# Performance work log

Measured on AMD Instinct MI355X. Metric: run time of the kernel, lower is better.

## Reference

```python
import jax, jax.numpy as jnp
import numpy as np

N, E, D, H, G, C = 100000, 1200000, 64, 64, 128, 10


def setup_inputs() -> dict:
    key = jax.random.key(0)
    ks = jax.random.split(key, 20)
    def lin(k, fin, fout):
        kw, kb = jax.random.split(k)
        s = 1.0 / np.sqrt(fin)
        return (jax.random.uniform(kw, (fin, fout), jnp.float32, -s, s),
                jax.random.uniform(kb, (fout,), jnp.float32, -s, s))
    w1a, b1a = lin(ks[0], D, H)
    w1b, b1b = lin(ks[1], H, H)
    w2a, b2a = lin(ks[2], H, H)
    w2b, b2b = lin(ks[3], H, H)
    w3a, b3a = lin(ks[4], H, H)
    w3b, b3b = lin(ks[5], H, H)
    wc, bc = lin(ks[6], H, C)
    x = jax.random.normal(ks[7], (N, D), jnp.float32)
    edge_index = jax.random.randint(ks[8], (2, E), 0, N, dtype=jnp.int32)
    batch = jnp.sort(jax.random.randint(ks[9], (N,), 0, G, dtype=jnp.int32))
    return {"x": x, "w1a": w1a, "b1a": b1a, "w1b": w1b, "b1b": b1b,
            "w2a": w2a, "b2a": b2a, "w2b": w2b, "b2b": b2b,
            "w3a": w3a, "b3a": b3a, "w3b": w3b, "b3b": b3b,
            "wc": wc, "bc": bc, "edge_index": edge_index, "batch": batch}


def _gin_layer(x, src, dst, wa, ba, wb, bb):
    # GINConv (eps=0): mlp(x + sum_{j in N(i)} x_j), then outer ReLU from GIN.forward
    agg = jax.ops.segment_sum(x[src], dst, num_segments=N)  # [N, d]
    h = x + agg
    h = jax.nn.relu(h @ wa + ba) @ wb + bb
    return jax.nn.relu(h)


def reference(x, w1a, b1a, w1b, b1b, w2a, b2a, w2b, b2b,
              w3a, b3a, w3b, b3b, wc, bc, edge_index, batch):
    src, dst = edge_index[0], edge_index[1]
    x = _gin_layer(x, src, dst, w1a, b1a, w1b, b1b)
    x = _gin_layer(x, src, dst, w2a, b2a, w2b, b2b)
    x = _gin_layer(x, src, dst, w3a, b3a, w3b, b3b)
    # global mean pool over graphs
    sums = jax.ops.segment_sum(x, batch, num_segments=G)              # [G, H]
    cnts = jax.ops.segment_sum(jnp.ones((N,), x.dtype), batch, num_segments=G)
    pooled = sums / jnp.maximum(cnts, 1.0)[:, None]
    return pooled @ wc + bc  # [G, C]
```

## Files before the change

### kernel.cpp

```cpp
#include <hip/hip_runtime.h>
#include <hip/hip_bf16.h>


#define N_NODES 100000
#define N_EDGES 1200000
#define N_GRAPH 128
#define N_CLS   10
#define NBUCK   391
#define BCAP    4096
#define BSH     12

typedef __bf16 bf16_t;
typedef __bf16 bf16x8 __attribute__((ext_vector_type(8)));
typedef float  f32x4  __attribute__((ext_vector_type(4)));

__global__ void tobf_kernel(const float* __restrict__ x, bf16_t* __restrict__ xb,
                            int* __restrict__ bcnt, float* __restrict__ gsum,
                            const float* __restrict__ w1a, const float* __restrict__ w1b,
                            const float* __restrict__ w2a, const float* __restrict__ w2b,
                            const float* __restrict__ w3a, const float* __restrict__ w3b,
                            bf16_t* __restrict__ wfragG,
                            bf16_t* __restrict__ hPad, bf16_t* __restrict__ xAPad) {
    const int tid = threadIdx.x;
    if (blockIdx.x == 0) {
        for (int i = tid; i < NBUCK; i += 256) bcnt[i] = 0;
    } else if (blockIdx.x == 1) {
        f32x4* g4 = (f32x4*)gsum;
        for (int i = tid; i < N_GRAPH * 16; i += 256)
            g4[i] = (f32x4){0.f, 0.f, 0.f, 0.f};
        if (tid < 64) {
            xb[N_NODES * 64 + tid]    = (bf16_t)0.f;
            hPad[N_NODES * 64 + tid]  = (bf16_t)0.f;
            xAPad[N_NODES * 64 + tid] = (bf16_t)0.f;
        }
    } else if (blockIdx.x <= 4) {
        const int L = blockIdx.x - 2;
        const float* wA = L == 0 ? w1a : (L == 1 ? w2a : w3a);
        const float* wB = L == 0 ? w1b : (L == 1 ? w2b : w3b);
        const int k  = tid >> 2;
        const int n0 = (tid & 3) << 4;
        const int ks = k >> 5, qd = (k >> 3) & 3, jj = k & 7;
        const int fi = ((n0 >> 4) << 1) + ks;
#pragma unroll
        for (int m = 0; m < 2; ++m) {
            const float* w = m ? wB : wA;
            const f32x4 v0 = *(const f32x4*)(w + k * 64 + n0);
            const f32x4 v1 = *(const f32x4*)(w + k * 64 + n0 + 4);
            const f32x4 v2 = *(const f32x4*)(w + k * 64 + n0 + 8);
            const f32x4 v3 = *(const f32x4*)(w + k * 64 + n0 + 12);
            bf16_t* dst = wfragG + ((L * 2 + m) * 8 + fi) * 512 + jj;
#pragma unroll
            for (int l = 0; l < 4; ++l) {
                dst[(qd * 16 + l) * 8]      = (bf16_t)v0[l];
                dst[(qd * 16 + 4 + l) * 8]  = (bf16_t)v1[l];
                dst[(qd * 16 + 8 + l) * 8]  = (bf16_t)v2[l];
                dst[(qd * 16 + 12 + l) * 8] = (bf16_t)v3[l];
            }
        }
    }
    const int i = (blockIdx.x * 256 + tid) * 8;
    const f32x4 a = *(const f32x4*)(x + i);
    const f32x4 b = *(const f32x4*)(x + i + 4);
    bf16x8 o;
#pragma unroll
    for (int j = 0; j < 4; ++j) { o[j] = (bf16_t)a[j]; o[4 + j] = (bf16_t)b[j]; }
    *(bf16x8*)(xb + i) = o;
}

__global__ void binA_kernel(const int* __restrict__ ei,
                            int* __restrict__ bcnt,
                            int* __restrict__ bpair) {
    __shared__ int lcnt[NBUCK];
    __shared__ int lbase[NBUCK];
    const int t = threadIdx.x;
    for (int b = t; b < NBUCK; b += 256) lcnt[b] = 0;
    __syncthreads();
    const int e0 = (blockIdx.x * 256 + t) * 4;
    int4 s4, d4; int b[4], r[4];
    const bool valid = e0 < N_EDGES;
    if (valid) {
        s4 = *(const int4*)(ei + e0);
        d4 = *(const int4*)(ei + N_EDGES + e0);
        b[0] = d4.x >> 8; b[1] = d4.y >> 8; b[2] = d4.z >> 8; b[3] = d4.w >> 8;
        r[0] = atomicAdd(&lcnt[b[0]], 1);
        r[1] = atomicAdd(&lcnt[b[1]], 1);
        r[2] = atomicAdd(&lcnt[b[2]], 1);
        r[3] = atomicAdd(&lcnt[b[3]], 1);
    }
    __syncthreads();
    for (int bb = t; bb < NBUCK; bb += 256) {
        const int c = lcnt[bb];
        lbase[bb] = c ? atomicAdd(&bcnt[bb], c) : 0;
    }
    __syncthreads();
    if (valid) {
        const int ss[4] = {s4.x, s4.y, s4.z, s4.w};
        const int dd[4] = {d4.x, d4.y, d4.z, d4.w};
#pragma unroll
        for (int j = 0; j < 4; ++j) {
            const int slot = lbase[b[j]] + r[j];
            if (slot < BCAP)
                bpair[(b[j] << BSH) + slot] = (ss[j] << 8) | (dd[j] & 255);
        }
    }
}

__global__ void sortfill_kernel(const int* __restrict__ bpair,
                                const int* __restrict__ bcnt,
                                int* __restrict__ offset, int* __restrict__ csr) {
    __shared__ int red[256];
    __shared__ int hist[256];
    __shared__ int l[256];
    __shared__ int cursor[256];
    const int b = blockIdx.x;
    const int t = threadIdx.x;
    const int base = b << BSH;

    int part = 0;
    for (int i = t; i < b; i += 256) {
        int c = bcnt[i];
        part += (c < BCAP ? c : BCAP);
    }
    red[t] = part;
    __syncthreads();
    for (int d = 128; d > 0; d >>= 1) {
        if (t < d) red[t] += red[t + d];
        __syncthreads();
    }
    const int cbase = red[0];
    int cnt = bcnt[b];
    cnt = cnt < BCAP ? cnt : BCAP;
    if (b == NBUCK - 1 && t == 0) offset[N_NODES] = cbase + cnt;
    __syncthreads();

    hist[t] = 0;
    __syncthreads();
    for (int i = t; i < cnt; i += 256)
        atomicAdd(&hist[bpair[base + i] & 255], 1);
    __syncthreads();

    const int v = hist[t];
    l[t] = v;
    __syncthreads();
    for (int d = 1; d < 256; d <<= 1) {
        int u = l[t];
        if (t >= d) u += l[t - d];
        __syncthreads();
        l[t] = u;
        __syncthreads();
    }
    const int gpos = cbase + l[t] - v;
    const int node = (b << 8) + t;
    if (node < N_NODES) offset[node] = gpos;
    cursor[t] = gpos;
    __syncthreads();

    for (int i = t; i < cnt; i += 256) {
        const int p = bpair[base + i];
        const int pos = atomicAdd(&cursor[p & 255], 1);
        csr[pos] = p >> 8;
    }
}

#define G8(S, J, ACC)                                                          \
    {                                                                          \
        const int t0 = __shfl(S, (J) + 0), t1 = __shfl(S, (J) + 1);            \
        const int t2 = __shfl(S, (J) + 2), t3 = __shfl(S, (J) + 3);            \
        const int t4 = __shfl(S, (J) + 4), t5 = __shfl(S, (J) + 5);            \
        const int t6 = __shfl(S, (J) + 6), t7 = __shfl(S, (J) + 7);            \
        const float u0 = (float)x[t0 * 64 + f], u1 = (float)x[t1 * 64 + f];    \
        const float u2 = (float)x[t2 * 64 + f], u3 = (float)x[t3 * 64 + f];    \
        const float u4 = (float)x[t4 * 64 + f], u5 = (float)x[t5 * 64 + f];    \
        const float u6 = (float)x[t6 * 64 + f], u7 = (float)x[t7 * 64 + f];    \
        ACC += ((u0 + u1) + (u2 + u3)) + ((u4 + u5) + (u6 + u7));              \
    }

#define PRELOAD1(OV, X, SX)                                                    \
    {                                                                          \
        const int o_ = __shfl(OV, X);                                          \
        const int d_ = __shfl(OV, (X) + 1) - o_;                               \
        const int c_ = d_ < 64 ? d_ : 64;                                      \
        SX = N_NODES;                                                          \
        if (f < c_) SX = csr[o_ + f];                                          \
    }
#define PRELOAD8(OV, S0_, S1_, S2_, S3_, S4_, S5_, S6_, S7_)                   \
    PRELOAD1(OV, 0, S0_) PRELOAD1(OV, 1, S1_) PRELOAD1(OV, 2, S2_)             \
    PRELOAD1(OV, 3, S3_) PRELOAD1(OV, 4, S4_) PRELOAD1(OV, 5, S5_)             \
    PRELOAD1(OV, 6, S6_) PRELOAD1(OV, 7, S7_)

#define ROWPAIR(I, OV, SA, SB, R0W)                                            \
    {                                                                          \
        const int oA = __shfl(OV, I),     eA = __shfl(OV, (I) + 1);            \
        const int oB = __shfl(OV, (I) + 4), eB = __shfl(OV, (I) + 5);          \
        const int dA = eA - oA, dB = eB - oB;                                  \
        const int cA = dA < 64 ? dA : 64, cB = dB < 64 ? dB : 64;              \
        float accA = (float)x[((R0W) + I) * 64 + f];                           \
        float accB = (float)x[((R0W) + I + 4) * 64 + f];                       \
        const int cmax = cA > cB ? cA : cB;                                    \
        for (int j = 0; j < cmax; j += 8) {                                    \
            if (j < cA) { G8(SA, j, accA) }                                    \
            if (j < cB) { G8(SB, j, accB) }                                    \
        }                                                                      \
        if (dA > 64 || dB > 64) {                          \
            for (int base = 64; base < dA || base < dB; base += 64) {          \
                const int ra = dA - base, rb2 = dB - base;                     \
                const int ca2 = ra <= 0 ? 0 : (ra < 64 ? ra : 64);             \
                const int cb2 = rb2 <= 0 ? 0 : (rb2 < 64 ? rb2 : 64);          \
                int sA2 = N_NODES, sB2 = N_NODES;                              \
                if (f < ca2) sA2 = csr[oA + base + f];                         \
                if (f < cb2) sB2 = csr[oB + base + f];                         \
                const int cm2 = ca2 > cb2 ? ca2 : cb2;                         \
                for (int j = 0; j < cm2; j += 8) {                             \
                    if (j < ca2) { G8(sA2, j, accA) }                          \
                    if (j < cb2) { G8(sB2, j, accB) }                          \
                }                                                              \
            }                                                                  \
        }                                                                      \
        hs[half * 8 + I][lane]     = (bf16_t)accA;                             \
        hs[half * 8 + I + 4][lane] = (bf16_t)accB;                             \
    }

#define GEMM1_BODY                                                             \
    {                                                                          \
        bf16x8 af[2];                                                          \
        _Pragma("unroll")                                                      \
        for (int ks = 0; ks < 2; ++ks)                                         \
            af[ks] = *(const bf16x8*)(&hs[l15][ks * 32 + quad * 8]);           \
        _Pragma("unroll")                                                      \
        for (int c = 0; c < 2; ++c) {                                          \
            const int ct = half * 2 + c;                                       \
            const bf16x8 b0 = *(const bf16x8*)(wf + (ct * 2 + 0) * 512 + lane * 8); \
            const bf16x8 b1 = *(const bf16x8*)(wf + (ct * 2 + 1) * 512 + lane * 8); \
            f32x4 acc = {0.f, 0.f, 0.f, 0.f};                                  \
            acc = __builtin_amdgcn_mfma_f32_16x16x32_bf16(af[0], b0, acc, 0, 0, 0); \
            acc = __builtin_amdgcn_mfma_f32_16x16x32_bf16(af[1], b1, acc, 0, 0, 0); \
            const float bv = ba[ct * 16 + l15];                                \
            _Pragma("unroll")                                                  \
            for (int r = 0; r < 4; ++r) {                                      \
                float h = acc[r] + bv;                                         \
                h = h > 0.f ? h : 0.f;                                         \
                h2[quad * 4 + r][ct * 16 + l15] = (bf16_t)h;                   \
            }                                                                  \
        }                                                                      \
    }

#define GEMM2_BODY                                                             \
    {                                                                          \
        bf16x8 a2[2];                                                          \
        _Pragma("unroll")                                                      \
        for (int ks = 0; ks < 2; ++ks)                                         \
            a2[ks] = *(const bf16x8*)(&h2[l15][ks * 32 + quad * 8]);           \
        _Pragma("unroll")                                                      \
        for (int c = 0; c < 2; ++c) {                                          \
            const int ct = half * 2 + c;                                       \
            const bf16x8 b0 = *(const bf16x8*)(wf + (8 + ct * 2 + 0) * 512 + lane * 8); \
            const bf16x8 b1 = *(const bf16x8*)(wf + (8 + ct * 2 + 1) * 512 + lane * 8); \
            f32x4 acc = {0.f, 0.f, 0.f, 0.f};                                  \
            acc = __builtin_amdgcn_mfma_f32_16x16x32_bf16(a2[0], b0, acc, 0, 0, 0); \
            acc = __builtin_amdgcn_mfma_f32_16x16x32_bf16(a2[1], b1, acc, 0, 0, 0); \
            const float bv = bb[ct * 16 + l15];                                \
            _Pragma("unroll")                                                  \
            for (int r = 0; r < 4; ++r) {                                      \
                float h = acc[r] + bv;                                         \
                h = h > 0.f ? h : 0.f;                                         \
                hs[quad * 4 + r][ct * 16 + l15] = (bf16_t)h;                   \
            }                                                                  \
        }                                                                      \
    }

#define EPILOGUE(RB, R0W)                                                      \
    if (POOL) {                                                                \
        int cur = -1;                                                          \
        float acc = 0.f;                                                       \
        for (int r = 0; r < 8; ++r) {                                          \
            const int row = (R0W) + r;                                         \
            const int g = batch[row];                        \
            const float v = (float)hs[half * 8 + r][lane];                     \
            if (g != cur) {                                                    \
                if (cur >= 0) unsafeAtomicAdd(gsum + cur * 64 + lane, acc);    \
                acc = 0.f;                                                     \
                cur = g;                                                       \
            }                                                                  \
            acc += v;                                                          \
        }                                                                      \
        if (cur >= 0) unsafeAtomicAdd(gsum + cur * 64 + lane, acc);            \
    } else {                                                                   \
        const int row16 = half * 8 + (lane >> 3);                              \
        const int colg  = (lane & 7) * 8;                                      \
        const bf16x8 v = *(const bf16x8*)&hs[row16][colg];                     \
        *(bf16x8*)(xout + ((RB) + row16) * 64 + colg) = v;                     \
    }

template <int POOL>
__global__ void gmlp_kernel(const bf16_t* __restrict__ x,
                            const int* __restrict__ offset,
                            const int* __restrict__ csr,
                            const bf16_t* __restrict__ wf,
                            const float* __restrict__ ba, const float* __restrict__ bb,
                            bf16_t* __restrict__ xout,
                            const int* __restrict__ batch,
                            float* __restrict__ gsum) {
    __shared__ __align__(16) bf16_t hs[16][72];
    __shared__ __align__(16) bf16_t h2[16][72];

    const int tid  = threadIdx.x;
    const int half = tid >> 6;
    const int lane = tid & 63;
    const int l15  = lane & 15;
    const int quad = lane >> 4;
    const int f    = lane;

    const int rb0  = blockIdx.x * 32;
    const int rb1  = rb0 + 16;
    const int r0wA = rb0 + half * 8;
    const int r0wB = rb1 + half * 8;

    int offvA = 0;
    if (lane < 9) offvA = offset[r0wA + lane];
    int a0, a1, a2, a3, a4, a5, a6, a7;
    PRELOAD8(offvA, a0, a1, a2, a3, a4, a5, a6, a7)

    ROWPAIR(0, offvA, a0, a4, r0wA)
    ROWPAIR(1, offvA, a1, a5, r0wA)
    ROWPAIR(2, offvA, a2, a6, r0wA)
    ROWPAIR(3, offvA, a3, a7, r0wA)

    int offvB = 0;
    if (lane < 9) offvB = offset[r0wB + lane];

    __syncthreads();
    GEMM1_BODY

    int b0_, b1_, b2_, b3_, b4_, b5_, b6_, b7_;
    PRELOAD8(offvB, b0_, b1_, b2_, b3_, b4_, b5_, b6_, b7_)

    __syncthreads();
    GEMM2_BODY
    __syncthreads();
    EPILOGUE(rb0, r0wA)

    __syncthreads();

    ROWPAIR(0, offvB, b0_, b4_, r0wB)
    ROWPAIR(1, offvB, b1_, b5_, r0wB)
    ROWPAIR(2, offvB, b2_, b6_, r0wB)
    ROWPAIR(3, offvB, b3_, b7_, r0wB)

    __syncthreads();
    GEMM1_BODY
    __syncthreads();
    GEMM2_BODY
    __syncthreads();
    EPILOGUE(rb1, r0wB)
}

__global__ void cls_kernel(const float* __restrict__ gsum,
                           const int* __restrict__ batch,
                           const float* __restrict__ wc, const float* __restrict__ bc,
                           float* __restrict__ out) {
    const int g = blockIdx.x;
    const int c = threadIdx.x;
    if (c >= N_CLS) return;
    int lo = 0, hi = N_NODES;
    while (lo < hi) { const int m = (lo + hi) >> 1; if (batch[m] < g) lo = m + 1; else hi = m; }
    const int lb = lo;
    lo = 0; hi = N_NODES;
    while (lo < hi) { const int m = (lo + hi) >> 1; if (batch[m] <= g) lo = m + 1; else hi = m; }
    const int cnt = lo - lb;
    const float inv = 1.f / (float)(cnt > 1 ? cnt : 1);
    float acc = bc[c];
    for (int k = 0; k < 64; ++k)
        acc += gsum[g * 64 + k] * inv * wc[k * N_CLS + c];
    out[g * N_CLS + c] = acc;
}

extern "C" void kernel_launch(void* const* d_in, const int* in_sizes, int n_in,
                              void* d_out, int out_size, void* d_ws, size_t ws_size,
                              hipStream_t stream) {
    const float* x   = (const float*)d_in[0];
    const float* w1a = (const float*)d_in[1];
    const float* b1a = (const float*)d_in[2];
    const float* w1b = (const float*)d_in[3];
    const float* b1b = (const float*)d_in[4];
    const float* w2a = (const float*)d_in[5];
    const float* b2a = (const float*)d_in[6];
    const float* w2b = (const float*)d_in[7];
    const float* b2b = (const float*)d_in[8];
    const float* w3a = (const float*)d_in[9];
    const float* b3a = (const float*)d_in[10];
    const float* w3b = (const float*)d_in[11];
    const float* b3b = (const float*)d_in[12];
    const float* wc  = (const float*)d_in[13];
    const float* bc  = (const float*)d_in[14];
    const int*   ei    = (const int*)d_in[15];
    const int*   batch = (const int*)d_in[16];
    float* out = (float*)d_out;

    char*   ws     = (char*)d_ws;
    int*    bcnt   = (int*)ws;
    int*    offset = (int*)(ws + 3136);
    int*    csr    = (int*)(ws + 403152);
    int*    bpair  = (int*)(ws + 5203152);
    bf16_t* xbf    = (bf16_t*)(ws + 11609296);
    bf16_t* h      = (bf16_t*)(ws + 24409424);
    bf16_t* xA     = (bf16_t*)(ws + 37209552);
    float*  gsum   = (float*)(ws + 50009680);
    bf16_t* wfragG = (bf16_t*)(ws + 50042448);

    const int e4grid = (N_EDGES / 4 + 255) / 256;
    const int tiles2 = N_NODES / 32;

    tobf_kernel<<<(N_NODES * 64) / (256 * 8), 256, 0, stream>>>(
        x, xbf, bcnt, gsum, w1a, w1b, w2a, w2b, w3a, w3b, wfragG, h, xA);

    binA_kernel<<<e4grid, 256, 0, stream>>>(ei, bcnt, bpair);
    sortfill_kernel<<<NBUCK, 256, 0, stream>>>(bpair, bcnt, offset, csr);

    gmlp_kernel<0><<<tiles2, 128, 0, stream>>>(xbf, offset, csr, wfragG,         b1a, b1b, xA, nullptr, nullptr);
    gmlp_kernel<0><<<tiles2, 128, 0, stream>>>(xA,  offset, csr, wfragG + 8192,  b2a, b2b, h,  nullptr, nullptr);
    gmlp_kernel<1><<<tiles2, 128, 0, stream>>>(h,   offset, csr, wfragG + 16384, b3a, b3b, nullptr, batch, gsum);

    cls_kernel<<<N_GRAPH, 64, 0, stream>>>(gsum, batch, wc, bc, out);
}
```

Before: 329.3 us.

## Use persistent blocks with atomic tile counter for dynamic load balancing in GIN layers

```diff
diff --git a/kernel.cpp b/kernel.cpp
--- a/kernel.cpp
+++ b/kernel.cpp
@@ -9,6 +9,8 @@
 #define NBUCK   391
 #define BCAP    4096
 #define BSH     12
+#define NTILES  6250
+#define GRID_P  4096
 
 typedef __bf16 bf16_t;
 typedef __bf16 bf16x8 __attribute__((ext_vector_type(8)));
@@ -20,10 +22,12 @@
                             const float* __restrict__ w2a, const float* __restrict__ w2b,
                             const float* __restrict__ w3a, const float* __restrict__ w3b,
                             bf16_t* __restrict__ wfragG,
-                            bf16_t* __restrict__ hPad, bf16_t* __restrict__ xAPad) {
+                            bf16_t* __restrict__ hPad, bf16_t* __restrict__ xAPad,
+                            int* __restrict__ ctr) {
     const int tid = threadIdx.x;
     if (blockIdx.x == 0) {
         for (int i = tid; i < NBUCK; i += 256) bcnt[i] = 0;
+        if (tid < 3) ctr[tid] = GRID_P;
     } else if (blockIdx.x == 1) {
         f32x4* g4 = (f32x4*)gsum;
         for (int i = tid; i < N_GRAPH * 16; i += 256)
@@ -190,7 +194,7 @@
 
 #define ROWPAIR(I, OV, SA, SB, R0W)                                            \
     {                                                                          \
-        const int oA = __shfl(OV, I),     eA = __shfl(OV, (I) + 1);            \
+        const int oA = __shfl(OV, I),       eA = __shfl(OV, (I) + 1);          \
         const int oB = __shfl(OV, (I) + 4), eB = __shfl(OV, (I) + 5);          \
         const int dA = eA - oA, dB = eB - oB;                                  \
         const int cA = dA < 64 ? dA : 64, cB = dB < 64 ? dB : 64;              \
@@ -299,9 +303,11 @@
                             const float* __restrict__ ba, const float* __restrict__ bb,
                             bf16_t* __restrict__ xout,
                             const int* __restrict__ batch,
-                            float* __restrict__ gsum) {
+                            float* __restrict__ gsum,
+                            int* __restrict__ ctr) {
     __shared__ __align__(16) bf16_t hs[16][72];
     __shared__ __align__(16) bf16_t h2[16][72];
+    __shared__ int tsh;
 
     const int tid  = threadIdx.x;
     const int half = tid >> 6;
@@ -310,48 +316,48 @@
     const int quad = lane >> 4;
     const int f    = lane;
 
-    const int rb0  = blockIdx.x * 32;
-    const int rb1  = rb0 + 16;
-    const int r0wA = rb0 + half * 8;
-    const int r0wB = rb1 + half * 8;
-
-    int offvA = 0;
-    if (lane < 9) offvA = offset[r0wA + lane];
+    int tile = blockIdx.x;
+    int offv = 0;
+    if (lane < 9) offv = offset[tile * 16 + half * 8 + lane];
     int a0, a1, a2, a3, a4, a5, a6, a7;
-    PRELOAD8(offvA, a0, a1, a2, a3, a4, a5, a6, a7)
-
-    ROWPAIR(0, offvA, a0, a4, r0wA)
-    ROWPAIR(1, offvA, a1, a5, r0wA)
-    ROWPAIR(2, offvA, a2, a6, r0wA)
-    ROWPAIR(3, offvA, a3, a7, r0wA)
-
-    int offvB = 0;
-    if (lane < 9) offvB = offset[r0wB + lane];
-
-    __syncthreads();
-    GEMM1_BODY
-
-    int b0_, b1_, b2_, b3_, b4_, b5_, b6_, b7_;
-    PRELOAD8(offvB, b0_, b1_, b2_, b3_, b4_, b5_, b6_, b7_)
-
-    __syncthreads();
-    GEMM2_BODY
-    __syncthreads();
-    EPILOGUE(rb0, r0wA)
-
-    __syncthreads();
-
-    ROWPAIR(0, offvB, b0_, b4_, r0wB)
-    ROWPAIR(1, offvB, b1_, b5_, r0wB)
-    ROWPAIR(2, offvB, b2_, b6_, r0wB)
-    ROWPAIR(3, offvB, b3_, b7_, r0wB)
-
-    __syncthreads();
-    GEMM1_BODY
-    __syncthreads();
-    GEMM2_BODY
-    __syncthreads();
-    EPILOGUE(rb1, r0wB)
+    PRELOAD8(offv, a0, a1, a2, a3, a4, a5, a6, a7)
+
+    for (;;) {
+        const int rb  = tile * 16;
+        const int r0w = rb + half * 8;
+
+        if (tid == 0) tsh = atomicAdd(ctr, 1);
+
+        ROWPAIR(0, offv, a0, a4, r0w)
+        ROWPAIR(1, offv, a1, a5, r0w)
+        ROWPAIR(2, offv, a2, a6, r0w)
+        ROWPAIR(3, offv, a3, a7, r0w)
+
+        __syncthreads();
+
+        const int nt  = tsh;
+        const bool has = nt < NTILES;
+        int offvN = 0;
+        if (has && lane < 9) offvN = offset[nt * 16 + half * 8 + lane];
+
+        GEMM1_BODY
+
+        int b0_, b1_, b2_, b3_, b4_, b5_, b6_, b7_;
+        PRELOAD8(offvN, b0_, b1_, b2_, b3_, b4_, b5_, b6_, b7_)
+
+        __syncthreads();
+        GEMM2_BODY
+        __syncthreads();
+        EPILOGUE(rb, r0w)
+
+        if (!has) break;
+        __syncthreads();
+
+        tile = nt;
+        offv = offvN;
+        a0 = b0_; a1 = b1_; a2 = b2_; a3 = b3_;
+        a4 = b4_; a5 = b5_; a6 = b6_; a7 = b7_;
+    }
 }
 
 __global__ void cls_kernel(const float* __restrict__ gsum,
@@ -406,19 +412,19 @@
     bf16_t* xA     = (bf16_t*)(ws + 37209552);
     float*  gsum   = (float*)(ws + 50009680);
     bf16_t* wfragG = (bf16_t*)(ws + 50042448);
+    int*    ctr    = (int*)(ws + 50091600);
 
     const int e4grid = (N_EDGES / 4 + 255) / 256;
-    const int tiles2 = N_NODES / 32;
 
     tobf_kernel<<<(N_NODES * 64) / (256 * 8), 256, 0, stream>>>(
-        x, xbf, bcnt, gsum, w1a, w1b, w2a, w2b, w3a, w3b, wfragG, h, xA);
+        x, xbf, bcnt, gsum, w1a, w1b, w2a, w2b, w3a, w3b, wfragG, h, xA, ctr);
 
     binA_kernel<<<e4grid, 256, 0, stream>>>(ei, bcnt, bpair);
     sortfill_kernel<<<NBUCK, 256, 0, stream>>>(bpair, bcnt, offset, csr);
 
-    gmlp_kernel<0><<<tiles2, 128, 0, stream>>>(xbf, offset, csr, wfragG,         b1a, b1b, xA, nullptr, nullptr);
-    gmlp_kernel<0><<<tiles2, 128, 0, stream>>>(xA,  offset, csr, wfragG + 8192,  b2a, b2b, h,  nullptr, nullptr);
-    gmlp_kernel<1><<<tiles2, 128, 0, stream>>>(h,   offset, csr, wfragG + 16384, b3a, b3b, nullptr, batch, gsum);
+    gmlp_kernel<0><<<GRID_P, 128, 0, stream>>>(xbf, offset, csr, wfragG,         b1a, b1b, xA, nullptr, nullptr, ctr + 0);
+    gmlp_kernel<0><<<GRID_P, 128, 0, stream>>>(xA,  offset, csr, wfragG + 8192,  b2a, b2b, h,  nullptr, nullptr, ctr + 1);
+    gmlp_kernel<1><<<GRID_P, 128, 0, stream>>>(h,   offset, csr, wfragG + 16384, b3a, b3b, nullptr, batch, gsum, ctr + 2);
 
     cls_kernel<<<N_GRAPH, 64, 0, stream>>>(gsum, batch, wc, bc, out);
 }
```

Result: slower. 594.2 us (+80.5%).
